# Kernel tuning notes

Hardware: AMD Instinct MI355X
Metric: run time of the kernel (lower is better)

Reference implementation:

```python
import jax, jax.numpy as jnp
import numpy as np

D_MODEL = 1024
NUM_HEADS = 16
D_K = D_MODEL // NUM_HEADS


def setup_inputs() -> dict:
    key = jax.random.key(0)
    ks = jax.random.split(key, 8)
    B, S, D = 4, 2048, D_MODEL
    scale = 1.0 / np.sqrt(D)
    return {
        "query": jax.random.normal(ks[0], (B, S, D), dtype=jnp.float32),
        "key": jax.random.normal(ks[1], (B, S, D), dtype=jnp.float32),
        "value": jax.random.normal(ks[2], (B, S, D), dtype=jnp.float32),
        "Wq": jax.random.normal(ks[3], (D, D), dtype=jnp.float32) * scale,
        "bq": jnp.zeros((D,), dtype=jnp.float32),
        "Wk": jax.random.normal(ks[4], (D, D), dtype=jnp.float32) * scale,
        "bk": jnp.zeros((D,), dtype=jnp.float32),
        "Wv": jax.random.normal(ks[5], (D, D), dtype=jnp.float32) * scale,
        "bv": jnp.zeros((D,), dtype=jnp.float32),
        "Wo": jax.random.normal(ks[6], (D, D), dtype=jnp.float32) * scale,
        "bo": jnp.zeros((D,), dtype=jnp.float32),
    }


def reference(query, key, value, Wq, bq, Wk, bk, Wv, bv, Wo, bo):
    B, S, D = query.shape
    H, dk = NUM_HEADS, D_K

    def proj(x, W, b):
        # nn.Linear: x @ W.T + b, then split heads -> [B, H, S, dk]
        y = jnp.einsum("bsd,ed->bse", x, W) + b
        return y.reshape(B, -1, H, dk).transpose(0, 2, 1, 3)

    Q = proj(query, Wq, bq)
    K = proj(key, Wk, bk)
    V = proj(value, Wv, bv)

    scores = jnp.einsum("bhqd,bhkd->bhqk", Q, K) / np.sqrt(dk).astype(jnp.float32)
    attn = jax.nn.softmax(scores, axis=-1)
    out = jnp.einsum("bhqk,bhkd->bhqd", attn, V)  # [B, H, S, dk]
    out = out.transpose(0, 2, 1, 3).reshape(B, -1, D)
    return jnp.einsum("bsd,ed->bse", out, Wo) + bo
```

## Files before the change

### kernel.cpp

```cpp
#include <hip/hip_runtime.h>
#include <hip/hip_bf16.h>

typedef unsigned short u16;
typedef __attribute__((ext_vector_type(8))) short bf16x8;
typedef __attribute__((ext_vector_type(4))) short bf16x4;
typedef __attribute__((ext_vector_type(4))) float f32x4;

#define LOG2E_OVER8 0.18033688011112043f

__device__ __forceinline__ float ex2(float x) {
#if __has_builtin(__builtin_amdgcn_exp2f)
    return __builtin_amdgcn_exp2f(x);
#else
    float r;
    asm volatile("v_exp_f32 %0, %1" : "=v"(r) : "v"(x));
    return r;
#endif
}

__device__ __forceinline__ u16 f2bf(float f) {
    unsigned u = __float_as_uint(f);
    u += 0x7FFFu + ((u >> 16) & 1u);
    return (u16)(u >> 16);
}

__device__ __forceinline__ unsigned pk_rtz(float lo, float hi) {
    return __builtin_amdgcn_perm(__float_as_uint(hi), __float_as_uint(lo), 0x07060302u);
}
__device__ __forceinline__ bf16x8 pack8(float a0, float a1, float a2, float a3,
                                        float a4, float a5, float a6, float a7) {
    unsigned p[4];
    p[0] = pk_rtz(a0, a1);
    p[1] = pk_rtz(a2, a3);
    p[2] = pk_rtz(a4, a5);
    p[3] = pk_rtz(a6, a7);
    bf16x8 r;
    __builtin_memcpy(&r, p, 16);
    return r;
}

__device__ __forceinline__ f32x4 mfma32(bf16x8 a, bf16x8 b, f32x4 c) {
    return __builtin_amdgcn_mfma_f32_16x16x32_bf16(a, b, c, 0, 0, 0);
}

__device__ __forceinline__ void gload16(const void* g, void* l) {
    __builtin_amdgcn_global_load_lds((const __attribute__((address_space(1))) unsigned int*)g,
                                     (__attribute__((address_space(3))) unsigned int*)l,
                                     16, 0, 0);
}

__global__ __launch_bounds__(256) void cvt_all(const float* __restrict__ q, const float* __restrict__ k,
                                               const float* __restrict__ v, const float* __restrict__ wq,
                                               const float* __restrict__ wk, const float* __restrict__ wv,
                                               const float* __restrict__ wo, u16* __restrict__ xout,
                                               u16* __restrict__ wout) {
    const int bid = blockIdx.x;
    const float* src;
    u16* dst;
    size_t off;
    if (bid < 24576) {
        const int t = bid >> 13, c = bid & 8191;
        src = (t == 0) ? q : (t == 1) ? k : v;
        dst = xout + (size_t)t * (8192ull * 1024);
        off = (size_t)c * 1024 + threadIdx.x * 4;
    } else {
        const int t = (bid - 24576) >> 10, c = (bid - 24576) & 1023;
        src = (t == 0) ? wq : (t == 1) ? wk : (t == 2) ? wv : wo;
        dst = wout + (size_t)t * (1024ull * 1024);
        off = (size_t)c * 1024 + threadIdx.x * 4;
    }
    float4 val = *(const float4*)(src + off);
    bf16x4 o;
    o[0] = (short)f2bf(val.x); o[1] = (short)f2bf(val.y);
    o[2] = (short)f2bf(val.z); o[3] = (short)f2bf(val.w);
    *(bf16x4*)(dst + off) = o;
}

struct GemmAcc { f32x4 a[4][4]; };

__device__ __forceinline__ void gemm_core(const u16* __restrict__ A, const u16* __restrict__ Bt,
                                          u16* As, u16* Bs, int bm, int bn, GemmAcc& acc) {
    constexpr int K = 1024;
    const int tid = threadIdx.x;
    const int lane = tid & 63;
    const int lr = lane & 15, lg = lane >> 4;
    const int l7 = lr & 7;

    for (int i = 0; i < 4; i++)
        for (int j = 0; j < 4; j++) acc.a[i][j] = (f32x4){0.f, 0.f, 0.f, 0.f};

    const int row0 = tid >> 3, u0 = tid & 7;
    const int su = (u0 ^ (row0 & 7)) * 8;
    size_t a_off[4], b_off[4];
#pragma unroll
    for (int i = 0; i < 4; i++) {
        a_off[i] = (size_t)(bm + i * 32 + row0) * K + su;
        b_off[i] = (size_t)(bn + i * 32 + row0) * K + su;
    }
    const int c0 = tid * 8;

    const int wid = tid >> 6, wr = wid >> 1, wc = wid & 1;

    for (int kt = 0; kt < K; kt += 64) {
#pragma unroll
        for (int i = 0; i < 4; i++) gload16(A + a_off[i] + kt, &As[i * 2048 + c0]);
#pragma unroll
        for (int i = 0; i < 4; i++) gload16(Bt + b_off[i] + kt, &Bs[i * 2048 + c0]);
        __syncthreads();
#pragma unroll
        for (int kh = 0; kh < 2; kh++) {
            const int fu = ((kh * 4 + lg) ^ l7) * 8;
            bf16x8 aF[4], bF[4];
#pragma unroll
            for (int mi = 0; mi < 4; mi++) aF[mi] = *(const bf16x8*)&As[(wr * 64 + mi * 16 + lr) * 64 + fu];
#pragma unroll
            for (int ni = 0; ni < 4; ni++) bF[ni] = *(const bf16x8*)&Bs[(wc * 64 + ni * 16 + lr) * 64 + fu];
#pragma unroll
            for (int mi = 0; mi < 4; mi++)
#pragma unroll
                for (int ni = 0; ni < 4; ni++) acc.a[mi][ni] = mfma32(aF[mi], bF[ni], acc.a[mi][ni]);
        }
        __syncthreads();
    }
}

template<int MODE>
__global__ __launch_bounds__(256) void gemm_bt(const u16* __restrict__ A, const u16* __restrict__ Bt,
                                               const float* __restrict__ bias, void* __restrict__ Cout,
                                               float scale) {
    __shared__ u16 As[128 * 64];
    __shared__ u16 Bs[128 * 64];
    const int bid = blockIdx.x;
    const int m_ = bid & 63, n_ = bid >> 6;
    const int bm = m_ * 128, bn = n_ * 128;
    GemmAcc acc;
    gemm_core(A, Bt, As, Bs, bm, bn, acc);

    const int lane = threadIdx.x & 63, wid = threadIdx.x >> 6;
    const int wr = wid >> 1, wc = wid & 1;
    const int lr = lane & 15, lg = lane >> 4;

#pragma unroll
    for (int ni = 0; ni < 4; ni++) {
        const int n = bn + wc * 64 + ni * 16 + lr;
        const float bv = bias[n];
#pragma unroll
        for (int mi = 0; mi < 4; mi++) {
            const int mbase = bm + wr * 64 + mi * 16 + lg * 4;
#pragma unroll
            for (int r = 0; r < 4; r++) {
                const int m = mbase + r;
                const float v = acc.a[mi][ni][r] + bv;
                if (MODE == 0) {
                    ((float*)Cout)[(size_t)m * 1024 + n] = v;
                } else if (MODE == 1) {
                    ((u16*)Cout)[(size_t)m * 1024 + n] = f2bf(v * scale);
                } else {
                    const int bq_ = m >> 11, kk = m & 2047, kb = kk >> 6, k64 = kk & 63;
                    const int hh = n >> 6, dd = n & 63;
                    const int ks = k64 >> 4, g = (k64 >> 2) & 3, rr = k64 & 3;
                    const int unit = ((ks >> 1) << 2) | g;
                    const int jj = ((ks & 1) << 2) | rr;
                    ((u16*)Cout)[((size_t)((bq_ * 16 + hh) * 32 + kb)) * 4096 +
                                 dd * 64 + ((unit ^ (dd & 7)) << 3) + jj] = f2bf(v);
                }
            }
        }
    }
}

__global__ __launch_bounds__(256, 2) void attn_fwd(const u16* __restrict__ Qp, const u16* __restrict__ Kp,
                                                   const u16* __restrict__ VTb, u16* __restrict__ AO) {
    __shared__ u16 kt[2][4096];
    __shared__ u16 vt[2][4096];
    const int tid = threadIdx.x;
    const int lane = tid & 63, wave = tid >> 6;
    const int lr = lane & 15, lg = lane >> 4;
    const int l7 = lr & 7;
    const int bh = blockIdx.x & 63, b = bh >> 4, h = bh & 15;
    const int q0 = (blockIdx.x >> 6) * 256 + wave * 64;

    const u16* qbase = Qp + (size_t)(b * 2048 + q0) * 1024 + h * 64;
    bf16x8 qf[4][2];
#pragma unroll
    for (int qt = 0; qt < 4; qt++)
#pragma unroll
        for (int hf = 0; hf < 2; hf++)
            qf[qt][hf] = *(const bf16x8*)(qbase + (size_t)(qt * 16 + lr) * 1024 + hf * 32 + lg * 8);

    const int srow = tid >> 3;
    const int scol = (((tid & 7) ^ (srow & 7)) * 8);
    const u16* kg = Kp + (size_t)(b * 2048 + srow) * 1024 + h * 64 + scol;
    const u16* vg = VTb + (size_t)(b * 16 + h) * 32 * 4096 + tid * 8;
    const int ldst = tid * 8;

#define STAGE(buf, kb_)                                                       \
    do {                                                                      \
        gload16(kg + (size_t)(kb_) * 64 * 1024,        &kt[buf][ldst]);       \
        gload16(kg + (size_t)((kb_) * 64 + 32) * 1024, &kt[buf][2048 + ldst]);\
        gload16(vg + (size_t)(kb_) * 4096,             &vt[buf][ldst]);       \
        gload16(vg + (size_t)(kb_) * 4096 + 2048,      &vt[buf][2048 + ldst]);\
    } while (0)

    f32x4 lsacc[4];
    f32x4 ot[4][4];
#pragma unroll
    for (int qt = 0; qt < 4; qt++) {
        lsacc[qt] = (f32x4){0.f, 0.f, 0.f, 0.f};
#pragma unroll
        for (int dt = 0; dt < 4; dt++) ot[qt][dt] = (f32x4){0.f, 0.f, 0.f, 0.f};
    }

    bf16x8 ones8;
#pragma unroll
    for (int i = 0; i < 8; i++) ones8[i] = (short)0x3F80;

    STAGE(0, 0);
    __syncthreads();
    int cur = 0;

    const f32x4 zero = (f32x4){0.f, 0.f, 0.f, 0.f};
    const int ku0 = (lg ^ l7) * 8;
    const int ku1 = ((4 + lg) ^ l7) * 8;

#pragma unroll 2
    for (int it = 0; it < 32; ++it) {
        if (it < 31) STAGE(cur ^ 1, it + 1);

        const u16* kl = &kt[cur][0];
        const u16* vl = &vt[cur][0];

        f32x4 s[4][4];
        __builtin_amdgcn_s_setprio(1);
#pragma unroll
        for (int ks = 0; ks < 4; ++ks) {
            const int rbase = (ks * 16 + lr) * 64;
            bf16x8 kf0 = *(const bf16x8*)&kl[rbase + ku0];
            bf16x8 kf1 = *(const bf16x8*)&kl[rbase + ku1];
#pragma unroll
            for (int qt = 0; qt < 4; ++qt) {
                s[qt][ks] = mfma32(kf0, qf[qt][0], zero);
                s[qt][ks] = mfma32(kf1, qf[qt][1], s[qt][ks]);
            }
        }
        __builtin_amdgcn_s_setprio(0);

        bf16x8 pf[4][2];
#pragma unroll
        for (int qt = 0; qt < 4; ++qt) {
#pragma unroll
            for (int kh = 0; kh < 2; ++kh) {
                const f32x4 sa = s[qt][2 * kh], sb = s[qt][2 * kh + 1];
                pf[qt][kh] = pack8(ex2(sa[0]), ex2(sa[1]), ex2(sa[2]), ex2(sa[3]),
                                   ex2(sb[0]), ex2(sb[1]), ex2(sb[2]), ex2(sb[3]));
                lsacc[qt] = mfma32(ones8, pf[qt][kh], lsacc[qt]);
            }
        }

        __builtin_amdgcn_s_setprio(1);
#pragma unroll
        for (int dt = 0; dt < 4; ++dt) {
            const int vrow = (dt * 16 + lr) * 64;
            bf16x8 vf0 = *(const bf16x8*)&vl[vrow + ku0];
            bf16x8 vf1 = *(const bf16x8*)&vl[vrow + ku1];
#pragma unroll
            for (int qt = 0; qt < 4; ++qt) {
                ot[qt][dt] = mfma32(vf0, pf[qt][0], ot[qt][dt]);
                ot[qt][dt] = mfma32(vf1, pf[qt][1], ot[qt][dt]);
            }
        }
        __builtin_amdgcn_s_setprio(0);

        __syncthreads();
        cur ^= 1;
    }

    float inv[4];
#pragma unroll
    for (int qt = 0; qt < 4; qt++) inv[qt] = 1.0f / lsacc[qt][0];
    u16* t_ = &kt[0][0] + wave * 2048;
#pragma unroll
    for (int pass = 0; pass < 2; ++pass) {
        __syncthreads();
#pragma unroll
        for (int qh = 0; qh < 2; ++qh) {
            const int qt = pass * 2 + qh;
#pragma unroll
            for (int dt = 0; dt < 4; ++dt)
#pragma unroll
                for (int r = 0; r < 4; ++r)
                    t_[(qh * 16 + lr) * 64 + dt * 16 + lg * 4 + r] = f2bf(ot[qt][dt][r] * inv[qt]);
        }
        __syncthreads();
        const int qq = lane >> 1, dseg = (lane & 1) * 32;
        u16* dst = AO + (size_t)(b * 2048 + q0 + pass * 32 + qq) * 1024 + h * 64 + dseg;
        bf16x8 o_[4];
#pragma unroll
        for (int j = 0; j < 4; ++j) o_[j] = *(const bf16x8*)&t_[qq * 64 + dseg + j * 8];
#pragma unroll
        for (int j = 0; j < 4; ++j) *(bf16x8*)(dst + j * 8) = o_[j];
    }
#undef STAGE
}

extern "C" void kernel_launch(void* const* d_in, const int* in_sizes, int n_in,
                              void* d_out, int out_size, void* d_ws, size_t ws_size,
                              hipStream_t stream) {
    const float* q_in = (const float*)d_in[0];
    const float* k_in = (const float*)d_in[1];
    const float* v_in = (const float*)d_in[2];
    const float* Wq = (const float*)d_in[3];
    const float* bq = (const float*)d_in[4];
    const float* Wk = (const float*)d_in[5];
    const float* bk = (const float*)d_in[6];
    const float* Wv = (const float*)d_in[7];
    const float* bv = (const float*)d_in[8];
    const float* Wo = (const float*)d_in[9];
    const float* bo = (const float*)d_in[10];

    const size_t MD = (size_t)8192 * 1024;
    const size_t DD = (size_t)1024 * 1024;
    u16* ws = (u16*)d_ws;
    u16* Xq = ws;
    u16* Xk = Xq + MD;
    u16* Xv = Xk + MD;
    u16* Wqb = Xq + 3 * MD;
    u16* Wkb = Wqb + DD;
    u16* Wvb = Wkb + DD;
    u16* Wob = Wvb + DD;
    u16* Qp = Wqb + 4 * DD;
    u16* Kp = Qp + MD;
    u16* VTb = Kp + MD;
    u16* AO = VTb + MD;

    cvt_all<<<28672, 256, 0, stream>>>(q_in, k_in, v_in, Wq, Wk, Wv, Wo, Xq, Wqb);

    gemm_bt<1><<<512, 256, 0, stream>>>(Xq, Wqb, bq, Qp, LOG2E_OVER8);
    gemm_bt<1><<<512, 256, 0, stream>>>(Xk, Wkb, bk, Kp, 1.0f);
    gemm_bt<2><<<512, 256, 0, stream>>>(Xv, Wvb, bv, VTb, 1.0f);

    attn_fwd<<<512, 256, 0, stream>>>(Qp, Kp, VTb, AO);

    gemm_bt<0><<<512, 256, 0, stream>>>(AO, Wob, bo, (float*)d_out, 1.0f);
}
```

Measured before the change: 190.9 us.

## Fuse fp32-to-bf16 activation conversion into projection GEMM A-tile loads

Removes the separate activation conversion kernel. The Q/K/V projection GEMMs now read fp32 inputs directly, round them to bf16 in registers and write them into swizzled LDS, with a register double-buffered prefetch of the next A tile. Only the weights are still converted by a small kernel. This is meant to eliminate the extra write and re-read of the bf16 activation copies. The cost is higher register pressure and synchronous global loads in the GEMM main loop, plus a rounding mode that differs slightly from round-to-nearest-even.

```diff
diff --git a/kernel.cpp b/kernel.cpp
--- a/kernel.cpp
+++ b/kernel.cpp
@@ -39,6 +39,12 @@
     return r;
 }
 
+__device__ __forceinline__ unsigned pk_rhu(float lo, float hi) {
+    unsigned a = __float_as_uint(lo) + 0x8000u;
+    unsigned b = __float_as_uint(hi) + 0x8000u;
+    return __builtin_amdgcn_perm(b, a, 0x07060302u);
+}
+
 __device__ __forceinline__ f32x4 mfma32(bf16x8 a, bf16x8 b, f32x4 c) {
     return __builtin_amdgcn_mfma_f32_16x16x32_bf16(a, b, c, 0, 0, 0);
 }
@@ -49,31 +55,16 @@
                                      16, 0, 0);
 }
 
-__global__ __launch_bounds__(256) void cvt_all(const float* __restrict__ q, const float* __restrict__ k,
-                                               const float* __restrict__ v, const float* __restrict__ wq,
-                                               const float* __restrict__ wk, const float* __restrict__ wv,
-                                               const float* __restrict__ wo, u16* __restrict__ xout,
-                                               u16* __restrict__ wout) {
-    const int bid = blockIdx.x;
-    const float* src;
-    u16* dst;
-    size_t off;
-    if (bid < 24576) {
-        const int t = bid >> 13, c = bid & 8191;
-        src = (t == 0) ? q : (t == 1) ? k : v;
-        dst = xout + (size_t)t * (8192ull * 1024);
-        off = (size_t)c * 1024 + threadIdx.x * 4;
-    } else {
-        const int t = (bid - 24576) >> 10, c = (bid - 24576) & 1023;
-        src = (t == 0) ? wq : (t == 1) ? wk : (t == 2) ? wv : wo;
-        dst = wout + (size_t)t * (1024ull * 1024);
-        off = (size_t)c * 1024 + threadIdx.x * 4;
-    }
-    float4 val = *(const float4*)(src + off);
+__global__ __launch_bounds__(256) void cvt_w4(const float* __restrict__ a, const float* __restrict__ b,
+                                              const float* __restrict__ c, const float* __restrict__ d,
+                                              u16* __restrict__ out) {
+    const float* src = (blockIdx.y == 0) ? a : (blockIdx.y == 1) ? b : (blockIdx.y == 2) ? c : d;
+    size_t i = ((size_t)blockIdx.x * 256 + threadIdx.x) * 4;
+    float4 v = *(const float4*)(src + i);
     bf16x4 o;
-    o[0] = (short)f2bf(val.x); o[1] = (short)f2bf(val.y);
-    o[2] = (short)f2bf(val.z); o[3] = (short)f2bf(val.w);
-    *(bf16x4*)(dst + off) = o;
+    o[0] = (short)f2bf(v.x); o[1] = (short)f2bf(v.y);
+    o[2] = (short)f2bf(v.z); o[3] = (short)f2bf(v.w);
+    *(bf16x4*)(out + (size_t)blockIdx.y * (1024ull * 1024) + i) = o;
 }
 
 struct GemmAcc { f32x4 a[4][4]; };
@@ -98,7 +89,6 @@
         b_off[i] = (size_t)(bn + i * 32 + row0) * K + su;
     }
     const int c0 = tid * 8;
-
     const int wid = tid >> 6, wr = wid >> 1, wc = wid & 1;
 
     for (int kt = 0; kt < K; kt += 64) {
@@ -125,9 +115,103 @@
 }
 
 template<int MODE>
-__global__ __launch_bounds__(256) void gemm_bt(const u16* __restrict__ A, const u16* __restrict__ Bt,
-                                               const float* __restrict__ bias, void* __restrict__ Cout,
-                                               float scale) {
+__global__ __launch_bounds__(256, 2) void gemm_f32a(const float* __restrict__ A, const u16* __restrict__ Bt,
+                                                    const float* __restrict__ bias, u16* __restrict__ Cout,
+                                                    float scale) {
+    __shared__ u16 As[128 * 64];
+    __shared__ u16 Bs[128 * 64];
+    const int tid = threadIdx.x;
+    const int bid = blockIdx.x;
+    const int m_ = bid & 63, n_ = bid >> 6;
+    const int bm = m_ * 128, bn = n_ * 128;
+    const int lane = tid & 63;
+    const int lr = lane & 15, lg = lane >> 4;
+    const int l7 = lr & 7;
+
+    f32x4 acc[4][4];
+    for (int i = 0; i < 4; i++)
+        for (int j = 0; j < 4; j++) acc[i][j] = (f32x4){0.f, 0.f, 0.f, 0.f};
+
+    const int row0 = tid >> 3, u0 = tid & 7;
+    const int su = (u0 ^ (row0 & 7)) * 8;
+    size_t b_off[4];
+#pragma unroll
+    for (int i = 0; i < 4; i++) b_off[i] = (size_t)(bn + i * 32 + row0) * 1024 + su;
+    const int c0 = tid * 8;
+
+    const int ar = tid >> 4;
+    const size_t a_base = (size_t)(bm + ar) * 1024 + (tid & 15) * 4;
+    const int wds = ar * 64 + ((((tid & 15) >> 1) ^ (ar & 7)) << 3) + (tid & 1) * 4;
+
+    float4 fA[2][8];
+#pragma unroll
+    for (int j = 0; j < 8; ++j) fA[0][j] = *(const float4*)(A + a_base + (size_t)j * 16384);
+
+    const int wid = tid >> 6, wr = wid >> 1, wc = wid & 1;
+
+#pragma unroll 2
+    for (int t = 0; t < 16; ++t) {
+        const int cur = t & 1;
+        const int kt = t * 64;
+#pragma unroll
+        for (int i = 0; i < 4; i++) gload16(Bt + b_off[i] + kt, &Bs[i * 2048 + c0]);
+        const int ktn = ((t + 1) & 15) * 64;
+#pragma unroll
+        for (int j = 0; j < 8; ++j) fA[cur ^ 1][j] = *(const float4*)(A + a_base + ktn + (size_t)j * 16384);
+#pragma unroll
+        for (int j = 0; j < 8; ++j) {
+            const float4 v = fA[cur][j];
+            unsigned p2[2];
+            p2[0] = pk_rhu(v.x, v.y);
+            p2[1] = pk_rhu(v.z, v.w);
+            __builtin_memcpy(&As[wds + j * 1024], p2, 8);
+        }
+        __syncthreads();
+#pragma unroll
+        for (int kh = 0; kh < 2; kh++) {
+            const int fu = ((kh * 4 + lg) ^ l7) * 8;
+            bf16x8 aF[4], bF[4];
+#pragma unroll
+            for (int mi = 0; mi < 4; mi++) aF[mi] = *(const bf16x8*)&As[(wr * 64 + mi * 16 + lr) * 64 + fu];
+#pragma unroll
+            for (int ni = 0; ni < 4; ni++) bF[ni] = *(const bf16x8*)&Bs[(wc * 64 + ni * 16 + lr) * 64 + fu];
+#pragma unroll
+            for (int mi = 0; mi < 4; mi++)
+#pragma unroll
+                for (int ni = 0; ni < 4; ni++) acc[mi][ni] = mfma32(aF[mi], bF[ni], acc[mi][ni]);
+        }
+        __syncthreads();
+    }
+
+#pragma unroll
+    for (int ni = 0; ni < 4; ni++) {
+        const int n = bn + wc * 64 + ni * 16 + lr;
+        const float bv = bias[n];
+#pragma unroll
+        for (int mi = 0; mi < 4; mi++) {
+            const int mbase = bm + wr * 64 + mi * 16 + lg * 4;
+#pragma unroll
+            for (int r = 0; r < 4; r++) {
+                const int m = mbase + r;
+                const float v = acc[mi][ni][r] + bv;
+                if (MODE == 1) {
+                    Cout[(size_t)m * 1024 + n] = f2bf(v * scale);
+                } else {
+                    const int bq_ = m >> 11, kk = m & 2047, kb = kk >> 6, k64 = kk & 63;
+                    const int hh = n >> 6, dd = n & 63;
+                    const int ks = k64 >> 4, g = (k64 >> 2) & 3, rr = k64 & 3;
+                    const int unit = ((ks >> 1) << 2) | g;
+                    const int jj = ((ks & 1) << 2) | rr;
+                    Cout[((size_t)((bq_ * 16 + hh) * 32 + kb)) * 4096 +
+                         dd * 64 + ((unit ^ (dd & 7)) << 3) + jj] = f2bf(v);
+                }
+            }
+        }
+    }
+}
+
+__global__ __launch_bounds__(256) void gemm_out(const u16* __restrict__ A, const u16* __restrict__ Bt,
+                                                const float* __restrict__ bias, float* __restrict__ Cout) {
     __shared__ u16 As[128 * 64];
     __shared__ u16 Bs[128 * 64];
     const int bid = blockIdx.x;
@@ -139,7 +223,6 @@
     const int lane = threadIdx.x & 63, wid = threadIdx.x >> 6;
     const int wr = wid >> 1, wc = wid & 1;
     const int lr = lane & 15, lg = lane >> 4;
-
 #pragma unroll
     for (int ni = 0; ni < 4; ni++) {
         const int n = bn + wc * 64 + ni * 16 + lr;
@@ -148,23 +231,8 @@
         for (int mi = 0; mi < 4; mi++) {
             const int mbase = bm + wr * 64 + mi * 16 + lg * 4;
 #pragma unroll
-            for (int r = 0; r < 4; r++) {
-                const int m = mbase + r;
-                const float v = acc.a[mi][ni][r] + bv;
-                if (MODE == 0) {
-                    ((float*)Cout)[(size_t)m * 1024 + n] = v;
-                } else if (MODE == 1) {
-                    ((u16*)Cout)[(size_t)m * 1024 + n] = f2bf(v * scale);
-                } else {
-                    const int bq_ = m >> 11, kk = m & 2047, kb = kk >> 6, k64 = kk & 63;
-                    const int hh = n >> 6, dd = n & 63;
-                    const int ks = k64 >> 4, g = (k64 >> 2) & 3, rr = k64 & 3;
-                    const int unit = ((ks >> 1) << 2) | g;
-                    const int jj = ((ks & 1) << 2) | rr;
-                    ((u16*)Cout)[((size_t)((bq_ * 16 + hh) * 32 + kb)) * 4096 +
-                                 dd * 64 + ((unit ^ (dd & 7)) << 3) + jj] = f2bf(v);
-                }
-            }
+            for (int r = 0; r < 4; r++)
+                Cout[(size_t)(mbase + r) * 1024 + n] = acc.a[mi][ni][r] + bv;
         }
     }
 }
@@ -321,10 +389,7 @@
     const size_t MD = (size_t)8192 * 1024;
     const size_t DD = (size_t)1024 * 1024;
     u16* ws = (u16*)d_ws;
-    u16* Xq = ws;
-    u16* Xk = Xq + MD;
-    u16* Xv = Xk + MD;
-    u16* Wqb = Xq + 3 * MD;
+    u16* Wqb = ws;
     u16* Wkb = Wqb + DD;
     u16* Wvb = Wkb + DD;
     u16* Wob = Wvb + DD;
@@ -333,13 +398,13 @@
     u16* VTb = Kp + MD;
     u16* AO = VTb + MD;
 
-    cvt_all<<<28672, 256, 0, stream>>>(q_in, k_in, v_in, Wq, Wk, Wv, Wo, Xq, Wqb);
-
-    gemm_bt<1><<<512, 256, 0, stream>>>(Xq, Wqb, bq, Qp, LOG2E_OVER8);
-    gemm_bt<1><<<512, 256, 0, stream>>>(Xk, Wkb, bk, Kp, 1.0f);
-    gemm_bt<2><<<512, 256, 0, stream>>>(Xv, Wvb, bv, VTb, 1.0f);
+    cvt_w4<<<dim3(1024, 4), 256, 0, stream>>>(Wq, Wk, Wv, Wo, Wqb);
+
+    gemm_f32a<1><<<512, 256, 0, stream>>>(q_in, Wqb, bq, Qp, LOG2E_OVER8);
+    gemm_f32a<1><<<512, 256, 0, stream>>>(k_in, Wkb, bk, Kp, 1.0f);
+    gemm_f32a<2><<<512, 256, 0, stream>>>(v_in, Wvb, bv, VTb, 1.0f);
 
     attn_fwd<<<512, 256, 0, stream>>>(Qp, Kp, VTb, AO);
 
-    gemm_bt<0><<<512, 256, 0, stream>>>(AO, Wob, bo, (float*)d_out, 1.0f);
-}
+    gemm_out<<<512, 256, 0, stream>>>(AO, Wob, bo, (float*)d_out);
+}
```

After: 183.0 us. 1.04x faster.
